# Performance work log

Hardware: AMD Instinct MI355X
Metric: run time of the kernel (lower is better)

## Reference

```python
import jax, jax.numpy as jnp
import numpy as np

T, B, I, H = 512, 64, 1024, 1024


def setup_inputs() -> dict:
    key = jax.random.key(0)
    ks = jax.random.split(key, 7)
    s = 1.0 / np.sqrt(H)  # torch LSTMCell default init scale
    return {
        "x": jax.random.normal(ks[0], (T, B, I), dtype=jnp.float32),
        "h0": jax.random.normal(ks[1], (B, H), dtype=jnp.float32),
        "c0": jax.random.normal(ks[2], (B, H), dtype=jnp.float32),
        "W_ih": jax.random.normal(ks[3], (4 * H, I), dtype=jnp.float32) * s,
        "W_hh": jax.random.normal(ks[4], (4 * H, H), dtype=jnp.float32) * s,
        "b_ih": jax.random.normal(ks[5], (4 * H,), dtype=jnp.float32) * s,
        "b_hh": jax.random.normal(ks[6], (4 * H,), dtype=jnp.float32) * s,
    }


def _reverse_lstm(x, h0, c0, W_ih, W_hh, b_ih, b_hh):
    def step(carry, x_t):
        h, c = carry
        # gates: [B, 4H]
        gates = x_t @ W_ih.T + b_ih + h @ W_hh.T + b_hh
        i_g, f_g, g_g, o_g = jnp.split(gates, 4, axis=-1)
        i_g = jax.nn.sigmoid(i_g)
        f_g = jax.nn.sigmoid(f_g)
        g_g = jnp.tanh(g_g)
        o_g = jax.nn.sigmoid(o_g)
        c_new = f_g * c + i_g * g_g
        h_new = o_g * jnp.tanh(c_new)
        return (h_new, c_new), h_new

    # reverse=True: scan from last timestep to first; ys[i] aligns with x[i],
    # matching the torch code's reverse(unbind) -> loop -> reverse(outputs).
    (hT, cT), ys = jax.lax.scan(step, (h0, c0), x, reverse=True)
    return ys, (hT, cT)


def reference(x, h0, c0, W_ih, W_hh, b_ih, b_hh):
    return _reverse_lstm(x, h0, c0, W_ih, W_hh, b_ih, b_hh)
```

## Files before the change

kernel.cpp:

```cpp
#include <hip/hip_runtime.h>

#define TT 512
#define BB 64
#define HH 1024
#define G4 4096

typedef _Float16 h8 __attribute__((ext_vector_type(8)));
typedef float f4 __attribute__((ext_vector_type(4)));
typedef unsigned long long u64;


__global__ void k_conv_wih(const float* __restrict__ w, _Float16* __restrict__ o) {
  int i = blockIdx.x * 256 + threadIdx.x;
  const f4* src = (const f4*)w + (size_t)i * 2;
  f4 a = src[0], b = src[1];
  h8 r;
  r[0] = (_Float16)a[0]; r[1] = (_Float16)a[1]; r[2] = (_Float16)a[2]; r[3] = (_Float16)a[3];
  r[4] = (_Float16)b[0]; r[5] = (_Float16)b[1]; r[6] = (_Float16)b[2]; r[7] = (_Float16)b[3];
  *(h8*)(o + (size_t)i * 8) = r;
}

__global__ void k_shuf_whh(const float* __restrict__ w, _Float16* __restrict__ o) {
  int cidx = blockIdx.x * 256 + threadIdx.x;
  int b = cidx >> 6;
  int lid = cidx & 63;
  int n = (b >> 5) * 16 + (lid & 15);
  int k0 = (b & 31) * 32 + (lid >> 4) * 8;
  const float* src = w + (size_t)n * HH + k0;
  h8 r;
  #pragma unroll
  for (int j = 0; j < 8; ++j) r[j] = (_Float16)src[j];
  *(h8*)(o + (size_t)b * 512 + lid * 8) = r;
}

__global__ void k_bsum(const float* __restrict__ bi, const float* __restrict__ bh,
                       float* __restrict__ o) {
  int i = blockIdx.x * 256 + threadIdx.x;
  o[i] = bi[i] + bh[i];
}

__global__ void k_prep(const float* __restrict__ h0, _Float16* __restrict__ hbuf,
                       unsigned* __restrict__ bar) {
  int i = blockIdx.x * 256 + threadIdx.x;
  hbuf[i] = (_Float16)h0[i];
  if (i < 2048) bar[i] = 0u;
}

__global__ __launch_bounds__(256) void k_gemm_gx(
    const float* __restrict__ x, const _Float16* __restrict__ wih,
    const float* __restrict__ bsum, _Float16* __restrict__ gx) {
  __shared__ _Float16 As[128 * 40];
  __shared__ _Float16 Bs[128 * 40];
  const int bid = blockIdx.x;
  const int m0 = (bid >> 5) * 128;
  const int n0 = (bid & 31) * 128;
  const int tid = threadIdx.x;
  const int w = tid >> 6, l = tid & 63, q = l >> 4, lj = l & 15;
  const int wm = (w >> 1) * 64, wn = (w & 1) * 64;
  const int lrow = tid >> 1;
  const int lcol = (tid & 1) * 16;

  f4 z = {0.f, 0.f, 0.f, 0.f};
  f4 acc[4][4];
  #pragma unroll
  for (int i2 = 0; i2 < 4; ++i2)
    #pragma unroll
    for (int j2 = 0; j2 < 4; ++j2) acc[i2][j2] = z;

  for (int kt = 0; kt < 32; ++kt) {
    const int k0 = kt * 32;
    const float* xp = x + (size_t)(m0 + lrow) * HH + k0 + lcol;
    f4 a0 = ((const f4*)xp)[0];
    f4 a1 = ((const f4*)xp)[1];
    f4 a2 = ((const f4*)xp)[2];
    f4 a3 = ((const f4*)xp)[3];
    const _Float16* bp = wih + (size_t)(n0 + lrow) * HH + k0 + lcol;
    h8 b0 = ((const h8*)bp)[0];
    h8 b1 = ((const h8*)bp)[1];
    h8 lo, hi;
    lo[0] = (_Float16)a0[0]; lo[1] = (_Float16)a0[1]; lo[2] = (_Float16)a0[2]; lo[3] = (_Float16)a0[3];
    lo[4] = (_Float16)a1[0]; lo[5] = (_Float16)a1[1]; lo[6] = (_Float16)a1[2]; lo[7] = (_Float16)a1[3];
    hi[0] = (_Float16)a2[0]; hi[1] = (_Float16)a2[1]; hi[2] = (_Float16)a2[2]; hi[3] = (_Float16)a2[3];
    hi[4] = (_Float16)a3[0]; hi[5] = (_Float16)a3[1]; hi[6] = (_Float16)a3[2]; hi[7] = (_Float16)a3[3];
    __syncthreads();
    *(h8*)&As[lrow * 40 + lcol] = lo;
    *(h8*)&As[lrow * 40 + lcol + 8] = hi;
    *(h8*)&Bs[lrow * 40 + lcol] = b0;
    *(h8*)&Bs[lrow * 40 + lcol + 8] = b1;
    __syncthreads();
    h8 af[4], bf[4];
    #pragma unroll
    for (int mt = 0; mt < 4; ++mt) af[mt] = *(h8*)&As[(wm + mt * 16 + lj) * 40 + q * 8];
    #pragma unroll
    for (int nt = 0; nt < 4; ++nt) bf[nt] = *(h8*)&Bs[(wn + nt * 16 + lj) * 40 + q * 8];
    #pragma unroll
    for (int mt = 0; mt < 4; ++mt)
      #pragma unroll
      for (int nt = 0; nt < 4; ++nt)
        acc[mt][nt] = __builtin_amdgcn_mfma_f32_16x16x32_f16(af[mt], bf[nt], acc[mt][nt], 0, 0, 0);
  }
  #pragma unroll
  for (int nt = 0; nt < 4; ++nt) {
    int n = n0 + wn + nt * 16 + lj;
    float bv = bsum[n];
    #pragma unroll
    for (int mt = 0; mt < 4; ++mt) {
      #pragma unroll
      for (int r = 0; r < 4; ++r) {
        int m = m0 + wm + mt * 16 + q * 4 + r;
        gx[(size_t)m * G4 + n] = (_Float16)(acc[mt][nt][r] + bv);
      }
    }
  }
}

__global__ __launch_bounds__(256, 1) void k_lstm_seq(
    const _Float16* __restrict__ gx, const _Float16* __restrict__ wsh,
    const float* __restrict__ c0, float* __restrict__ out,
    _Float16* __restrict__ hbuf, unsigned* __restrict__ bar) {
  __shared__ _Float16 hs[2][64 * 136];
  __shared__ float gbuf[4 * 64 * 20];
  __shared__ float cs[64 * 20];
  const int tid = threadIdx.x;
  const int s = blockIdx.x;
  const int w = tid >> 6;
  const int l = tid & 63;
  const int q = l >> 4;
  const int lj = l & 15;
  const int em = tid >> 2;
  const int ec = (tid & 3) * 4;

  #pragma unroll
  for (int u = 0; u < 4; ++u) {
    int e = u * 256 + tid;
    cs[(e >> 4) * 20 + (e & 15)] = c0[(size_t)(e >> 4) * HH + s * 16 + (e & 15)];
  }

  for (int ii = 0; ii < TT; ++ii) {
    const int t = TT - 1 - ii;
    const _Float16* __restrict__ hcur = hbuf + (size_t)(ii & 1) * (BB * HH);
    _Float16* __restrict__ hnxt = hbuf + (size_t)((ii + 1) & 1) * (BB * HH);
    const unsigned tgt = (unsigned)ii;

    const _Float16* gxb = gx + (size_t)t * BB * G4 + w * HH + s * 16;
    _Float16 gpre[16];
    #pragma unroll
    for (int mt = 0; mt < 4; ++mt)
      #pragma unroll
      for (int r = 0; r < 4; ++r)
        gpre[mt * 4 + r] = gxb[(size_t)(mt * 16 + q * 4 + r) * G4 + lj];

    u64 rdy = 0;
    auto wait_chunk = [&](int c) {
      while (((rdy >> (c * 8)) & 0xFFull) != 0xFFull) {
        unsigned v = __hip_atomic_load(&bar[l * 32], __ATOMIC_RELAXED,
                                       __HIP_MEMORY_SCOPE_AGENT);
        rdy = __ballot(v >= tgt);
        if (((rdy >> (c * 8)) & 0xFFull) == 0xFFull) break;
        __builtin_amdgcn_s_sleep(1);
      }
    };
    auto load_chunk = [&](int c, u64* dst) {
      #pragma unroll
      for (int u = 0; u < 8; ++u) {
        int e = u * 256 + tid;
        dst[u] = __hip_atomic_load(
            (const u64*)&hcur[(size_t)(e >> 5) * HH + c * 128 + (e & 31) * 4],
            __ATOMIC_RELAXED, __HIP_MEMORY_SCOPE_AGENT);
      }
    };

    f4 z = {0.f, 0.f, 0.f, 0.f};
    f4 acc[4];
    #pragma unroll
    for (int mt = 0; mt < 4; ++mt) acc[mt] = z;

    u64 pre0[8], pre1[8];
    wait_chunk(0); load_chunk(0, pre0);
    wait_chunk(1); load_chunk(1, pre1);

    #pragma unroll
    for (int ck = 0; ck < 8; ++ck) {
      u64* cur = (ck & 1) ? pre1 : pre0;
      #pragma unroll
      for (int u = 0; u < 8; ++u) {
        int e = u * 256 + tid;
        *(u64*)&hs[ck & 1][(e >> 5) * 136 + (e & 31) * 4] = cur[u];
      }
      __syncthreads();
      if (ck < 6) { wait_chunk(ck + 2); load_chunk(ck + 2, cur); }
      #pragma unroll
      for (int kk = 0; kk < 4; ++kk) {
        int blk = (w * 64 + s) * 32 + ck * 4 + kk;
        h8 bfr = *(const h8*)&wsh[(size_t)blk * 512 + l * 8];
        #pragma unroll
        for (int mt = 0; mt < 4; ++mt) {
          h8 afr = *(const h8*)&hs[ck & 1][(mt * 16 + lj) * 136 + kk * 32 + q * 8];
          acc[mt] = __builtin_amdgcn_mfma_f32_16x16x32_f16(afr, bfr, acc[mt], 0, 0, 0);
        }
      }
    }
    #pragma unroll
    for (int mt = 0; mt < 4; ++mt) {
      #pragma unroll
      for (int r = 0; r < 4; ++r) {
        int m = mt * 16 + q * 4 + r;
        gbuf[(w * 64 + m) * 20 + lj] = acc[mt][r] + (float)gpre[mt * 4 + r];
      }
    }
    __syncthreads();
    f4 gi4 = *(f4*)&gbuf[(0 * 64 + em) * 20 + ec];
    f4 gf4 = *(f4*)&gbuf[(1 * 64 + em) * 20 + ec];
    f4 gg4 = *(f4*)&gbuf[(2 * 64 + em) * 20 + ec];
    f4 go4 = *(f4*)&gbuf[(3 * 64 + em) * 20 + ec];
    f4 cold = *(f4*)&cs[em * 20 + ec];
    f4 hn4, cn4;
    #pragma unroll
    for (int j = 0; j < 4; ++j) {
      float iv = 1.f / (1.f + __expf(-gi4[j]));
      float fv = 1.f / (1.f + __expf(-gf4[j]));
      float gv = tanhf(gg4[j]);
      float ov = 1.f / (1.f + __expf(-go4[j]));
      float cn = fv * cold[j] + iv * gv;
      cn4[j] = cn;
      hn4[j] = ov * tanhf(cn);
    }
    *(f4*)&cs[em * 20 + ec] = cn4;
    union { _Float16 h[4]; u64 u; } pk;
    #pragma unroll
    for (int j = 0; j < 4; ++j) pk.h[j] = (_Float16)hn4[j];
    __hip_atomic_store((u64*)&hnxt[(size_t)em * HH + s * 16 + ec], pk.u,
                       __ATOMIC_RELAXED, __HIP_MEMORY_SCOPE_AGENT);
    *(f4*)&out[((size_t)t * BB + em) * HH + s * 16 + ec] = hn4;
    if (t == 0) {
      *(f4*)&out[(size_t)TT * BB * HH + (size_t)em * HH + s * 16 + ec] = hn4;
      *(f4*)&out[(size_t)TT * BB * HH + (size_t)BB * HH + (size_t)em * HH + s * 16 + ec] = cn4;
    }
    __syncthreads();
    if (tid == 0)
      __hip_atomic_store(&bar[s * 32], (unsigned)(ii + 1), __ATOMIC_RELAXED,
                         __HIP_MEMORY_SCOPE_AGENT);
  }
}

extern "C" void kernel_launch(void* const* d_in, const int* in_sizes, int n_in,
                              void* d_out, int out_size, void* d_ws, size_t ws_size,
                              hipStream_t stream) {
  const float* x    = (const float*)d_in[0];
  const float* h0   = (const float*)d_in[1];
  const float* c0   = (const float*)d_in[2];
  const float* W_ih = (const float*)d_in[3];
  const float* W_hh = (const float*)d_in[4];
  const float* b_ih = (const float*)d_in[5];
  const float* b_hh = (const float*)d_in[6];
  float* out = (float*)d_out;

  char* ws = (char*)d_ws;
  size_t off = 0;
  auto take = [&](size_t bytes) -> void* {
    void* p = ws + off;
    off = (off + bytes + 255) & ~(size_t)255;
    return p;
  };
  _Float16* gx    = (_Float16*)take((size_t)TT * BB * G4 * 2);
  _Float16* wih_h = (_Float16*)take((size_t)G4 * HH * 2);
  _Float16* wsh   = (_Float16*)take((size_t)G4 * HH * 2);
  float*    bsum  = (float*)take((size_t)G4 * 4);
  _Float16* hbuf  = (_Float16*)take((size_t)2 * BB * HH * 2);
  unsigned* bar   = (unsigned*)take(64 * 32 * 4);
  if (off > ws_size) return;

  k_conv_wih<<<2048, 256, 0, stream>>>(W_ih, wih_h);
  k_shuf_whh<<<2048, 256, 0, stream>>>(W_hh, wsh);
  k_bsum<<<16, 256, 0, stream>>>(b_ih, b_hh, bsum);
  k_prep<<<256, 256, 0, stream>>>(h0, hbuf, bar);
  k_gemm_gx<<<8192, 256, 0, stream>>>(x, wih_h, bsum, gx);
  k_lstm_seq<<<64, 256, 0, stream>>>(gx, wsh, c0, out, hbuf, bar);
}
```

Baseline: 4.840 ms.

## Reorder gx layout, stagger chunk order, deepen prefetch, and publish h before output stores

The gx GEMM now writes its results in a fragment-native layout, so each lane of the sequential LSTM kernel loads its gate preactivations with two vector loads instead of 16 scattered halves. Each block now starts its hidden-state chunk loop at a different chunk, uses a three-deep prefetch instead of two, and replaces __syncthreads with explicit waitcnt+barrier macros. The ready flag is published right after the h store is drained, before the big output stores, which shortens the critical path between steps. Gate activations use fast exp/rcp-based sigmoid and tanh, trading a little accuracy for fewer instructions.

```diff
diff --git a/kernel.cpp b/kernel.cpp
--- a/kernel.cpp
+++ b/kernel.cpp
@@ -8,6 +8,29 @@
 typedef _Float16 h8 __attribute__((ext_vector_type(8)));
 typedef float f4 __attribute__((ext_vector_type(4)));
 typedef unsigned long long u64;
+
+#define BAR_LGKM() do {                                      \
+  asm volatile("s_waitcnt lgkmcnt(0)" ::: "memory");         \
+  __builtin_amdgcn_sched_barrier(0);                         \
+  __builtin_amdgcn_s_barrier();                              \
+  __builtin_amdgcn_sched_barrier(0);                         \
+} while (0)
+
+#define BAR_VM0() do {                                       \
+  asm volatile("s_waitcnt vmcnt(0)" ::: "memory");           \
+  __builtin_amdgcn_sched_barrier(0);                         \
+  __builtin_amdgcn_s_barrier();                              \
+  __builtin_amdgcn_sched_barrier(0);                         \
+} while (0)
+
+__device__ __forceinline__ float sigm_fast(float x) {
+  return __builtin_amdgcn_rcpf(1.f + __expf(-x));
+}
+__device__ __forceinline__ float tanh_fast(float x) {
+  float cx = fminf(15.f, fmaxf(-15.f, x));
+  float e = __expf(2.f * cx);
+  return (e - 1.f) * __builtin_amdgcn_rcpf(e + 1.f);
+}
 
 
 __global__ void k_conv_wih(const float* __restrict__ w, _Float16* __restrict__ o) {
@@ -48,7 +71,7 @@
 
 __global__ __launch_bounds__(256) void k_gemm_gx(
     const float* __restrict__ x, const _Float16* __restrict__ wih,
-    const float* __restrict__ bsum, _Float16* __restrict__ gx) {
+    const float* __restrict__ bsum, _Float16* __restrict__ gxL) {
   __shared__ _Float16 As[128 * 40];
   __shared__ _Float16 Bs[128 * 40];
   const int bid = blockIdx.x;
@@ -99,23 +122,26 @@
       for (int nt = 0; nt < 4; ++nt)
         acc[mt][nt] = __builtin_amdgcn_mfma_f32_16x16x32_f16(af[mt], bf[nt], acc[mt][nt], 0, 0, 0);
   }
+  const int tt = (m0 + wm) >> 6;
   #pragma unroll
   for (int nt = 0; nt < 4; ++nt) {
-    int n = n0 + wn + nt * 16 + lj;
-    float bv = bsum[n];
+    int nbase = n0 + wn + nt * 16;
+    float bv = bsum[nbase + lj];
+    int wq = nbase >> 10;
+    int sq = (nbase >> 4) & 63;
+    _Float16* dst = gxL + (((size_t)tt * 4 + wq) * 64 + sq) * 1024 + (q * 16 + lj) * 16;
     #pragma unroll
     for (int mt = 0; mt < 4; ++mt) {
-      #pragma unroll
-      for (int r = 0; r < 4; ++r) {
-        int m = m0 + wm + mt * 16 + q * 4 + r;
-        gx[(size_t)m * G4 + n] = (_Float16)(acc[mt][nt][r] + bv);
-      }
+      union { _Float16 h[4]; u64 u; } pk;
+      #pragma unroll
+      for (int r = 0; r < 4; ++r) pk.h[r] = (_Float16)(acc[mt][nt][r] + bv);
+      *(u64*)(dst + mt * 4) = pk.u;
     }
   }
 }
 
 __global__ __launch_bounds__(256, 1) void k_lstm_seq(
-    const _Float16* __restrict__ gx, const _Float16* __restrict__ wsh,
+    const _Float16* __restrict__ gxL, const _Float16* __restrict__ wsh,
     const float* __restrict__ c0, float* __restrict__ out,
     _Float16* __restrict__ hbuf, unsigned* __restrict__ bar) {
   __shared__ _Float16 hs[2][64 * 136];
@@ -129,6 +155,7 @@
   const int lj = l & 15;
   const int em = tid >> 2;
   const int ec = (tid & 3) * 4;
+  const int c0r = s >> 3;
 
   #pragma unroll
   for (int u = 0; u < 4; ++u) {
@@ -142,13 +169,9 @@
     _Float16* __restrict__ hnxt = hbuf + (size_t)((ii + 1) & 1) * (BB * HH);
     const unsigned tgt = (unsigned)ii;
 
-    const _Float16* gxb = gx + (size_t)t * BB * G4 + w * HH + s * 16;
-    _Float16 gpre[16];
-    #pragma unroll
-    for (int mt = 0; mt < 4; ++mt)
-      #pragma unroll
-      for (int r = 0; r < 4; ++r)
-        gpre[mt * 4 + r] = gxb[(size_t)(mt * 16 + q * 4 + r) * G4 + lj];
+    const _Float16* gxb = gxL + (((size_t)t * 4 + w) * 64 + s) * 1024 + (size_t)l * 16;
+    h8 g0 = *(const h8*)gxb;
+    h8 g1 = *(const h8*)(gxb + 8);
 
     u64 rdy = 0;
     auto wait_chunk = [&](int c) {
@@ -175,23 +198,29 @@
     #pragma unroll
     for (int mt = 0; mt < 4; ++mt) acc[mt] = z;
 
-    u64 pre0[8], pre1[8];
-    wait_chunk(0); load_chunk(0, pre0);
-    wait_chunk(1); load_chunk(1, pre1);
+    u64 pre[3][8];
+    wait_chunk(c0r);             load_chunk(c0r, pre[0]);
+    wait_chunk((c0r + 1) & 7);   load_chunk((c0r + 1) & 7, pre[1]);
+    wait_chunk((c0r + 2) & 7);   load_chunk((c0r + 2) & 7, pre[2]);
 
     #pragma unroll
     for (int ck = 0; ck < 8; ++ck) {
-      u64* cur = (ck & 1) ? pre1 : pre0;
+      const int ckx = (ck + c0r) & 7;
+      u64* cur = pre[ck % 3];
       #pragma unroll
       for (int u = 0; u < 8; ++u) {
         int e = u * 256 + tid;
         *(u64*)&hs[ck & 1][(e >> 5) * 136 + (e & 31) * 4] = cur[u];
       }
-      __syncthreads();
-      if (ck < 6) { wait_chunk(ck + 2); load_chunk(ck + 2, cur); }
+      BAR_LGKM();
+      if (ck < 5) {
+        int cn = (ck + 3 + c0r) & 7;
+        wait_chunk(cn);
+        load_chunk(cn, cur);
+      }
       #pragma unroll
       for (int kk = 0; kk < 4; ++kk) {
-        int blk = (w * 64 + s) * 32 + ck * 4 + kk;
+        int blk = (w * 64 + s) * 32 + ckx * 4 + kk;
         h8 bfr = *(const h8*)&wsh[(size_t)blk * 512 + l * 8];
         #pragma unroll
         for (int mt = 0; mt < 4; ++mt) {
@@ -205,10 +234,11 @@
       #pragma unroll
       for (int r = 0; r < 4; ++r) {
         int m = mt * 16 + q * 4 + r;
-        gbuf[(w * 64 + m) * 20 + lj] = acc[mt][r] + (float)gpre[mt * 4 + r];
-      }
-    }
-    __syncthreads();
+        float gxv = (float)((mt < 2 ? g0 : g1)[(mt & 1) * 4 + r]);
+        gbuf[(w * 64 + m) * 20 + lj] = acc[mt][r] + gxv;
+      }
+    }
+    BAR_LGKM();
     f4 gi4 = *(f4*)&gbuf[(0 * 64 + em) * 20 + ec];
     f4 gf4 = *(f4*)&gbuf[(1 * 64 + em) * 20 + ec];
     f4 gg4 = *(f4*)&gbuf[(2 * 64 + em) * 20 + ec];
@@ -217,13 +247,13 @@
     f4 hn4, cn4;
     #pragma unroll
     for (int j = 0; j < 4; ++j) {
-      float iv = 1.f / (1.f + __expf(-gi4[j]));
-      float fv = 1.f / (1.f + __expf(-gf4[j]));
-      float gv = tanhf(gg4[j]);
-      float ov = 1.f / (1.f + __expf(-go4[j]));
+      float iv = sigm_fast(gi4[j]);
+      float fv = sigm_fast(gf4[j]);
+      float gv = tanh_fast(gg4[j]);
+      float ov = sigm_fast(go4[j]);
       float cn = fv * cold[j] + iv * gv;
       cn4[j] = cn;
-      hn4[j] = ov * tanhf(cn);
+      hn4[j] = ov * tanh_fast(cn);
     }
     *(f4*)&cs[em * 20 + ec] = cn4;
     union { _Float16 h[4]; u64 u; } pk;
@@ -231,15 +261,15 @@
     for (int j = 0; j < 4; ++j) pk.h[j] = (_Float16)hn4[j];
     __hip_atomic_store((u64*)&hnxt[(size_t)em * HH + s * 16 + ec], pk.u,
                        __ATOMIC_RELAXED, __HIP_MEMORY_SCOPE_AGENT);
+    BAR_VM0();
+    if (tid == 0)
+      __hip_atomic_store(&bar[s * 32], (unsigned)(ii + 1), __ATOMIC_RELAXED,
+                         __HIP_MEMORY_SCOPE_AGENT);
     *(f4*)&out[((size_t)t * BB + em) * HH + s * 16 + ec] = hn4;
     if (t == 0) {
       *(f4*)&out[(size_t)TT * BB * HH + (size_t)em * HH + s * 16 + ec] = hn4;
       *(f4*)&out[(size_t)TT * BB * HH + (size_t)BB * HH + (size_t)em * HH + s * 16 + ec] = cn4;
     }
-    __syncthreads();
-    if (tid == 0)
-      __hip_atomic_store(&bar[s * 32], (unsigned)(ii + 1), __ATOMIC_RELAXED,
-                         __HIP_MEMORY_SCOPE_AGENT);
   }
 }
 
@@ -262,7 +292,7 @@
     off = (off + bytes + 255) & ~(size_t)255;
     return p;
   };
-  _Float16* gx    = (_Float16*)take((size_t)TT * BB * G4 * 2);
+  _Float16* gxL   = (_Float16*)take((size_t)TT * BB * G4 * 2);
   _Float16* wih_h = (_Float16*)take((size_t)G4 * HH * 2);
   _Float16* wsh   = (_Float16*)take((size_t)G4 * HH * 2);
   float*    bsum  = (float*)take((size_t)G4 * 4);
@@ -274,6 +304,6 @@
   k_shuf_whh<<<2048, 256, 0, stream>>>(W_hh, wsh);
   k_bsum<<<16, 256, 0, stream>>>(b_ih, b_hh, bsum);
   k_prep<<<256, 256, 0, stream>>>(h0, hbuf, bar);
-  k_gemm_gx<<<8192, 256, 0, stream>>>(x, wih_h, bsum, gx);
-  k_lstm_seq<<<64, 256, 0, stream>>>(gx, wsh, c0, out, hbuf, bar);
-}
+  k_gemm_gx<<<8192, 256, 0, stream>>>(x, wih_h, bsum, gxL);
+  k_lstm_seq<<<64, 256, 0, stream>>>(gxL, wsh, c0, out, hbuf, bar);
+}
```

Result: no change. 4.893 ms (+1.1%).
